# Optimization experiments

Hardware: AMD Instinct MI355X
Metric: run time of the kernel (lower is better)

The kernel has to match this reference:

```python
import jax, jax.numpy as jnp
import numpy as np

ENTITY_DIM = 128; REL_DIM = 128; D1 = 8; D2 = 16
NC = 32; K = 3
H_OUT = D1 - K + 1; W_OUT = D2 - K + 1
FEAT = NC * H_OUT * W_OUT            # 2688
NUM_ENT = 40943; NUM_REL = 474; B = 256; HID = 256
EPS = 1e-5


def _bn(x, axes):
    # torch BatchNorm train mode with default gamma=1, beta=0 (biased variance)
    m = x.mean(axes, keepdims=True)
    v = x.var(axes, keepdims=True)
    return (x - m) * jax.lax.rsqrt(v + EPS)


def setup_inputs() -> dict:
    key = jax.random.key(0)
    ks = jax.random.split(key, 12)
    s = lambda k, shp, fan: jax.random.normal(k, shp, jnp.float32) / np.float32(np.sqrt(fan))
    return {
        "e1": jax.random.randint(ks[0], (B,), 0, NUM_ENT),
        "r": jax.random.randint(ks[1], (B,), 0, NUM_REL),
        "entity_emb": s(ks[2], (NUM_ENT, ENTITY_DIM), ENTITY_DIM),
        "relation_emb": s(ks[3], (NUM_REL, REL_DIM), REL_DIM),
        "convw_w1": s(ks[4], (REL_DIM, HID), REL_DIM),
        "convw_w2": s(ks[5], (HID, NC * K * K), HID),
        "convb_w1": s(ks[6], (REL_DIM, HID), REL_DIM),
        "convb_w2": s(ks[7], (HID, NC), HID),
        "fcw_w1": s(ks[8], (REL_DIM, HID), REL_DIM),
        "fcw_w2": s(ks[9], (HID, FEAT * ENTITY_DIM), HID),
        "fcb_w1": s(ks[10], (REL_DIM, HID), REL_DIM),
        "fcb_w2": s(ks[11], (HID, ENTITY_DIM), HID),
        "b": jnp.zeros((NUM_ENT,), jnp.float32),
    }


def reference(e1, r, entity_emb, relation_emb,
              convw_w1, convw_w2, convb_w1, convb_w2,
              fcw_w1, fcw_w2, fcb_w1, fcb_w2, b):
    E1 = entity_emb[e1].reshape(B, 1, D1, D2)      # [B,1,8,16]
    R = relation_emb[r]                            # [B,128]
    E2 = entity_emb                                # [NUM_ENT,128]

    x = _bn(E1, (0, 2, 3))                         # bn0 over batch+spatial, 1 channel

    # ContextualParameterGenerator: Linear -> ReLU -> Linear (no bias, eval dropout)
    cpg = lambda w1, w2: jax.nn.relu(R @ w1) @ w2

    filt = cpg(convw_w1, convw_w2).reshape(B * NC, 1, K, K)   # per-sample conv filters
    cbias = cpg(convb_w1, convb_w2)                            # [B,NC]

    # per-sample conv2d as a grouped conv: groups=B, each group has 1 in-ch, NC out-ch
    out = jax.lax.conv_general_dilated(
        x.reshape(1, B, D1, D2), filt,
        window_strides=(1, 1), padding='VALID',
        feature_group_count=B,
        dimension_numbers=('NCHW', 'OIHW', 'NCHW'))           # [1,B*NC,6,14]
    X = out.reshape(B, NC, H_OUT, W_OUT) + cbias[:, :, None, None]
    X = jax.nn.relu(X).reshape(B, FEAT)

    fc_w = cpg(fcw_w1, fcw_w2).reshape(B, FEAT, ENTITY_DIM)   # per-sample FC weights
    X = jnp.einsum('ij,ijk->ik', X, fc_w) + cpg(fcb_w1, fcb_w2)

    X = jax.nn.relu(_bn(X, (0,)))                              # bn2 + relu
    return jax.nn.sigmoid(X @ E2.T + b)                        # [B,NUM_ENT]
```

## Files before the change

### kernel.cpp

```cpp
#include <hip/hip_runtime.h>
#include <cstdint>
#include <cstddef>

#define BATCH 256
#define ED 128
#define NC 32
#define HO 6
#define WO 14
#define FEAT 2688
#define HID 256
#define NE 40943
#define EPS 1e-5f
#define W2COLS 344064

typedef __attribute__((ext_vector_type(4))) float f32x4;
typedef __attribute__((ext_vector_type(8))) short short8;

__device__ __forceinline__ ushort f2bf(float f) {
    uint32_t u = __builtin_bit_cast(uint32_t, f);
    u = (u + 0x7FFFu + ((u >> 16) & 1u)) >> 16;
    return (ushort)u;
}

__global__ void k0_bn0(const int* __restrict__ e1, const float* __restrict__ emb,
                       float* __restrict__ stats) {
    __shared__ float s1[1024], s2[1024];
    int t = threadIdx.x;
    int i = t >> 2, p = (t & 3) * 32;
    const float* row = emb + (size_t)e1[i] * ED + p;
    float a = 0.f, b = 0.f;
#pragma unroll
    for (int q = 0; q < 32; ++q) { float v = row[q]; a += v; b += v * v; }
    s1[t] = a; s2[t] = b;
    __syncthreads();
    for (int s = 512; s > 0; s >>= 1) {
        if (t < s) { s1[t] += s1[t + s]; s2[t] += s2[t + s]; }
        __syncthreads();
    }
    if (t == 0) {
        float m = s1[0] / 32768.f;
        float v = s2[0] / 32768.f - m * m;
        stats[0] = m;
        stats[1] = rsqrtf(v + EPS);
    }
}

__global__ void k1_hidden(const int* __restrict__ r, const float* __restrict__ rel,
                          const float* __restrict__ w1a, const float* __restrict__ w1b,
                          const float* __restrict__ w1c, const float* __restrict__ w1d,
                          float* __restrict__ H) {
    int head = blockIdx.x >> 8;
    int i = blockIdx.x & 255;
    int u = threadIdx.x;
    __shared__ float R[128];
    if (u < 128) R[u] = rel[(size_t)r[i] * 128 + u];
    __syncthreads();
    const float* w1 = head == 0 ? w1a : head == 1 ? w1b : head == 2 ? w1c : w1d;
    float acc = 0.f;
#pragma unroll 8
    for (int d = 0; d < 128; ++d) acc += R[d] * w1[d * 256 + u];
    H[((size_t)head * 256 + i) * 256 + u] = fmaxf(acc, 0.f);
}

__global__ void k2_heads(const float* __restrict__ H,
                         const float* __restrict__ w2f, const float* __restrict__ w2b,
                         const float* __restrict__ w2fcb,
                         float* __restrict__ filt, float* __restrict__ cbias,
                         float* __restrict__ fcb) {
    int i = blockIdx.x;
    int t = threadIdx.x;
    __shared__ float h0[256], h1[256], h3[256];
    if (t < 256) {
        h0[t] = H[(size_t)(0 * 256 + i) * 256 + t];
        h1[t] = H[(size_t)(1 * 256 + i) * 256 + t];
        h3[t] = H[(size_t)(3 * 256 + i) * 256 + t];
    }
    __syncthreads();
    if (t < 288) {
        float a = 0.f;
#pragma unroll 8
        for (int u = 0; u < 256; ++u) a += h0[u] * w2f[u * 288 + t];
        filt[i * 288 + t] = a;
    } else if (t < 320) {
        int c = t - 288;
        float a = 0.f;
#pragma unroll 8
        for (int u = 0; u < 256; ++u) a += h1[u] * w2b[u * 32 + c];
        cbias[i * 32 + c] = a;
    } else if (t < 448) {
        int c = t - 320;
        float a = 0.f;
#pragma unroll 8
        for (int u = 0; u < 256; ++u) a += h3[u] * w2fcb[u * 128 + c];
        fcb[i * 128 + c] = a;
    }
}

__global__ void k3_conv(const int* __restrict__ e1, const float* __restrict__ emb,
                        const float* __restrict__ stats, const float* __restrict__ filt,
                        const float* __restrict__ cbias, ushort* __restrict__ Xc) {
    int i = blockIdx.x, t = threadIdx.x;
    __shared__ float x[128], f[288], cb[32];
    float mean = stats[0], rstd = stats[1];
    if (t < 128) x[t] = (emb[(size_t)e1[i] * 128 + t] - mean) * rstd;
    if (t < 32) cb[t] = cbias[i * 32 + t];
    for (int o = t; o < 288; o += 256) f[o] = filt[i * 288 + o];
    __syncthreads();
    for (int o = t; o < FEAT; o += 256) {
        int c = o / 84, rem = o % 84;
        int y = rem / 14, xw = rem % 14;
        float acc = cb[c];
        const float* fc = &f[c * 9];
#pragma unroll
        for (int dy = 0; dy < 3; ++dy)
#pragma unroll
            for (int dx = 0; dx < 3; ++dx)
                acc += x[(y + dy) * 16 + (xw + dx)] * fc[dy * 3 + dx];
        Xc[(size_t)i * FEAT + o] = f2bf(fmaxf(acc, 0.f));
    }
}

__global__ __launch_bounds__(512, 2) void k4_gemm(const ushort* __restrict__ Xc,
                                                  const float* __restrict__ W2,
                                                  float* __restrict__ T) {
    int h = blockIdx.x;
    int tid = threadIdx.x, lane = tid & 63, wave = tid >> 6;
    int l15 = lane & 15, l4 = lane >> 4;
    __shared__ __align__(16) ushort Bt[128 * 40];
    const float* Brow = W2 + (size_t)h * W2COLS;

    int kk = tid & 127;
    int jg = tid >> 7;

    f32x4 acc[2][8];
#pragma unroll
    for (int mt = 0; mt < 2; ++mt)
#pragma unroll
        for (int nt = 0; nt < 8; ++nt)
#pragma unroll
            for (int q = 0; q < 4; ++q) acc[mt][nt][q] = 0.f;

    float p[8];
#pragma unroll
    for (int q = 0; q < 8; ++q) p[q] = Brow[(size_t)(jg * 8 + q) * 128 + kk];

    for (int s = 0; s < 84; ++s) {
        __syncthreads();
        short8 w8;
#pragma unroll
        for (int q = 0; q < 8; ++q) w8[q] = (short)f2bf(p[q]);
        *(short8*)&Bt[kk * 40 + jg * 8] = w8;
        __syncthreads();
        if (s + 1 < 84) {
            int j0n = (s + 1) * 32;
#pragma unroll
            for (int q = 0; q < 8; ++q)
                p[q] = Brow[(size_t)(j0n + jg * 8 + q) * 128 + kk];
        }
        int j0 = s * 32;
        short8 bf[8];
#pragma unroll
        for (int nt = 0; nt < 8; ++nt)
            bf[nt] = *(const short8*)&Bt[(nt * 16 + l15) * 40 + l4 * 8];
        short8 af[2];
#pragma unroll
        for (int mt = 0; mt < 2; ++mt) {
            int i = wave * 32 + mt * 16 + l15;
            af[mt] = *(const short8*)(Xc + (size_t)i * FEAT + j0 + l4 * 8);
        }
#pragma unroll
        for (int mt = 0; mt < 2; ++mt)
#pragma unroll
            for (int nt = 0; nt < 8; ++nt)
                acc[mt][nt] = __builtin_amdgcn_mfma_f32_16x16x32_bf16(
                    af[mt], bf[nt], acc[mt][nt], 0, 0, 0);
    }
#pragma unroll
    for (int mt = 0; mt < 2; ++mt)
#pragma unroll
        for (int nt = 0; nt < 8; ++nt) {
            int row0 = wave * 32 + mt * 16 + l4 * 4;
            int col = nt * 16 + l15;
#pragma unroll
            for (int rr = 0; rr < 4; ++rr)
                T[((size_t)h * 256 + row0 + rr) * 128 + col] = acc[mt][nt][rr];
        }
}

__global__ void k5_stage2(const float* __restrict__ T, const float* __restrict__ Hfc,
                          const float* __restrict__ fcb, float* __restrict__ X) {
    int i = blockIdx.x, k = threadIdx.x;
    const float* hp = Hfc + (size_t)i * 256;
    const float* tp = T + (size_t)i * 128 + k;
    float acc = fcb[i * 128 + k];
#pragma unroll 8
    for (int h = 0; h < 256; ++h) acc += hp[h] * tp[(size_t)h * 32768];
    X[i * 128 + k] = acc;
}

__global__ void k6_bn2(const float* __restrict__ X, ushort* __restrict__ Xn) {
    int k = blockIdx.x;
    int i = threadIdx.x;
    __shared__ float s1[256], s2[256];
    float v = X[i * 128 + k];
    s1[i] = v; s2[i] = v * v;
    __syncthreads();
    for (int s = 128; s > 0; s >>= 1) {
        if (i < s) { s1[i] += s1[i + s]; s2[i] += s2[i + s]; }
        __syncthreads();
    }
    float m = s1[0] / 256.f;
    float var = s2[0] / 256.f - m * m;
    float rstd = rsqrtf(var + EPS);
    Xn[i * 128 + k] = f2bf(fmaxf((v - m) * rstd, 0.f));
}

__global__ __launch_bounds__(256) void k7_final(const ushort* __restrict__ Xn,
                                                const float* __restrict__ E2,
                                                const float* __restrict__ bias,
                                                float* __restrict__ out) {
    int eb = blockIdx.x * 64;
    int lane = threadIdx.x & 63, wave = threadIdx.x >> 6;
    int l15 = lane & 15, l4 = lane >> 4;
    int i0 = wave * 64;

    f32x4 acc[4][4];
#pragma unroll
    for (int mt = 0; mt < 4; ++mt)
#pragma unroll
        for (int nt = 0; nt < 4; ++nt)
#pragma unroll
            for (int q = 0; q < 4; ++q) acc[mt][nt][q] = 0.f;

#pragma unroll
    for (int ks = 0; ks < 4; ++ks) {
        int k0 = ks * 32 + l4 * 8;
        short8 a[4];
#pragma unroll
        for (int mt = 0; mt < 4; ++mt) {
            int i = i0 + mt * 16 + l15;
            a[mt] = *(const short8*)(Xn + (size_t)i * 128 + k0);
        }
        short8 b[4];
#pragma unroll
        for (int nt = 0; nt < 4; ++nt) {
            int e = eb + nt * 16 + l15;
            int ec = e < NE ? e : NE - 1;
            const float* rp = E2 + (size_t)ec * 128 + k0;
            short8 tv;
#pragma unroll
            for (int q = 0; q < 8; ++q) tv[q] = (short)f2bf(rp[q]);
            b[nt] = tv;
        }
#pragma unroll
        for (int mt = 0; mt < 4; ++mt)
#pragma unroll
            for (int nt = 0; nt < 4; ++nt)
                acc[mt][nt] = __builtin_amdgcn_mfma_f32_16x16x32_bf16(
                    a[mt], b[nt], acc[mt][nt], 0, 0, 0);
    }
#pragma unroll
    for (int nt = 0; nt < 4; ++nt) {
        int e = eb + nt * 16 + l15;
        bool ok = e < NE;
        float bb = bias[e < NE ? e : NE - 1];
#pragma unroll
        for (int mt = 0; mt < 4; ++mt) {
            int row0 = i0 + mt * 16 + l4 * 4;
#pragma unroll
            for (int rr = 0; rr < 4; ++rr) {
                float v = acc[mt][nt][rr] + bb;
                float sg = 1.f / (1.f + __expf(-v));
                if (ok) out[(size_t)(row0 + rr) * NE + e] = sg;
            }
        }
    }
}

extern "C" void kernel_launch(void* const* d_in, const int* in_sizes, int n_in,
                              void* d_out, int out_size, void* d_ws, size_t ws_size,
                              hipStream_t stream) {
    const int* e1 = (const int*)d_in[0];
    const int* r = (const int*)d_in[1];
    const float* emb = (const float*)d_in[2];
    const float* rel = (const float*)d_in[3];
    const float* convw_w1 = (const float*)d_in[4];
    const float* convw_w2 = (const float*)d_in[5];
    const float* convb_w1 = (const float*)d_in[6];
    const float* convb_w2 = (const float*)d_in[7];
    const float* fcw_w1 = (const float*)d_in[8];
    const float* fcw_w2 = (const float*)d_in[9];
    const float* fcb_w1 = (const float*)d_in[10];
    const float* fcb_w2 = (const float*)d_in[11];
    const float* bvec = (const float*)d_in[12];
    float* out = (float*)d_out;

    char* ws = (char*)d_ws;
    float* stats = (float*)(ws + 0);
    float* H = (float*)(ws + 256);
    float* filt = (float*)(ws + 1048832);
    float* cbias = (float*)(ws + 1343744);
    float* fcbv = (float*)(ws + 1376512);
    ushort* Xc = (ushort*)(ws + 1507584);
    float* T = (float*)(ws + 2883840);
    float* X = (float*)(ws + 36438272);
    ushort* Xn = (ushort*)(ws + 36569344);

    k0_bn0<<<1, 1024, 0, stream>>>(e1, emb, stats);
    k1_hidden<<<1024, 256, 0, stream>>>(r, rel, convw_w1, convb_w1, fcw_w1, fcb_w1, H);
    k2_heads<<<256, 512, 0, stream>>>(H, convw_w2, convb_w2, fcb_w2, filt, cbias, fcbv);
    k3_conv<<<256, 256, 0, stream>>>(e1, emb, stats, filt, cbias, Xc);
    k4_gemm<<<256, 512, 0, stream>>>(Xc, fcw_w2, T);
    k5_stage2<<<256, 128, 0, stream>>>(T, H + 2 * 65536, fcbv, X);
    k6_bn2<<<128, 256, 0, stream>>>(X, Xn);
    k7_final<<<640, 256, 0, stream>>>(Xn, emb, bvec, out);
}
```

Baseline: 642.1 us.

## Split k4 GEMM columns across two blocks with double-buffered LDS and deeper prefetch

The per-hidden-unit GEMM now launches two blocks per h, each handling 64 of the 128 output columns. This doubles the grid to 512 blocks so more of the GPU is filled. The B tile is double-buffered in LDS, which removes one barrier per iteration, and global loads of W2 are prefetched two steps ahead. Each block still reloads the full Xc activation tile, so A-side traffic doubles. The launch-bounds occupancy hint is raised, and a stage-2 loop gets a larger unroll.

```diff
diff --git a/kernel.cpp b/kernel.cpp
--- a/kernel.cpp
+++ b/kernel.cpp
@@ -15,6 +15,7 @@
 
 typedef __attribute__((ext_vector_type(4))) float f32x4;
 typedef __attribute__((ext_vector_type(8))) short short8;
+typedef __attribute__((ext_vector_type(4))) short short4v;
 
 __device__ __forceinline__ ushort f2bf(float f) {
     uint32_t u = __builtin_bit_cast(uint32_t, f);
@@ -120,48 +121,52 @@
     }
 }
 
-__global__ __launch_bounds__(512, 2) void k4_gemm(const ushort* __restrict__ Xc,
+__global__ __launch_bounds__(512, 4) void k4_gemm(const ushort* __restrict__ Xc,
                                                   const float* __restrict__ W2,
                                                   float* __restrict__ T) {
-    int h = blockIdx.x;
+    int h = blockIdx.x >> 1;
+    int kh = (blockIdx.x & 1) * 64;
     int tid = threadIdx.x, lane = tid & 63, wave = tid >> 6;
     int l15 = lane & 15, l4 = lane >> 4;
-    __shared__ __align__(16) ushort Bt[128 * 40];
-    const float* Brow = W2 + (size_t)h * W2COLS;
-
-    int kk = tid & 127;
-    int jg = tid >> 7;
-
-    f32x4 acc[2][8];
+    __shared__ __align__(16) ushort Bt[2][64 * 36];
+    const float* Brow = W2 + (size_t)h * W2COLS + kh;
+
+    int kk = tid & 63;
+    int jg = tid >> 6;
+    const float* src = Brow + (size_t)(jg * 4) * 128 + kk;
+
+    f32x4 acc[2][4];
 #pragma unroll
     for (int mt = 0; mt < 2; ++mt)
 #pragma unroll
-        for (int nt = 0; nt < 8; ++nt)
+        for (int nt = 0; nt < 4; ++nt)
 #pragma unroll
             for (int q = 0; q < 4; ++q) acc[mt][nt][q] = 0.f;
 
-    float p[8];
-#pragma unroll
-    for (int q = 0; q < 8; ++q) p[q] = Brow[(size_t)(jg * 8 + q) * 128 + kk];
+    float p0[4], p1[4];
+#pragma unroll
+    for (int q = 0; q < 4; ++q) p0[q] = src[(size_t)q * 128];
+#pragma unroll
+    for (int q = 0; q < 4; ++q) p1[q] = src[(size_t)(32 + q) * 128];
 
     for (int s = 0; s < 84; ++s) {
+        short4v w4;
+#pragma unroll
+        for (int q = 0; q < 4; ++q) w4[q] = (short)f2bf(p0[q]);
+        *(short4v*)&Bt[s & 1][kk * 36 + jg * 4] = w4;
         __syncthreads();
-        short8 w8;
-#pragma unroll
-        for (int q = 0; q < 8; ++q) w8[q] = (short)f2bf(p[q]);
-        *(short8*)&Bt[kk * 40 + jg * 8] = w8;
-        __syncthreads();
-        if (s + 1 < 84) {
-            int j0n = (s + 1) * 32;
-#pragma unroll
-            for (int q = 0; q < 8; ++q)
-                p[q] = Brow[(size_t)(j0n + jg * 8 + q) * 128 + kk];
+#pragma unroll
+        for (int q = 0; q < 4; ++q) p0[q] = p1[q];
+        if (s + 2 < 84) {
+            int jb = (s + 2) * 32;
+#pragma unroll
+            for (int q = 0; q < 4; ++q) p1[q] = src[(size_t)(jb + q) * 128];
         }
         int j0 = s * 32;
-        short8 bf[8];
-#pragma unroll
-        for (int nt = 0; nt < 8; ++nt)
-            bf[nt] = *(const short8*)&Bt[(nt * 16 + l15) * 40 + l4 * 8];
+        short8 bf[4];
+#pragma unroll
+        for (int nt = 0; nt < 4; ++nt)
+            bf[nt] = *(const short8*)&Bt[s & 1][(nt * 16 + l15) * 36 + l4 * 8];
         short8 af[2];
 #pragma unroll
         for (int mt = 0; mt < 2; ++mt) {
@@ -171,16 +176,16 @@
 #pragma unroll
         for (int mt = 0; mt < 2; ++mt)
 #pragma unroll
-            for (int nt = 0; nt < 8; ++nt)
+            for (int nt = 0; nt < 4; ++nt)
                 acc[mt][nt] = __builtin_amdgcn_mfma_f32_16x16x32_bf16(
                     af[mt], bf[nt], acc[mt][nt], 0, 0, 0);
     }
 #pragma unroll
     for (int mt = 0; mt < 2; ++mt)
 #pragma unroll
-        for (int nt = 0; nt < 8; ++nt) {
+        for (int nt = 0; nt < 4; ++nt) {
             int row0 = wave * 32 + mt * 16 + l4 * 4;
-            int col = nt * 16 + l15;
+            int col = kh + nt * 16 + l15;
 #pragma unroll
             for (int rr = 0; rr < 4; ++rr)
                 T[((size_t)h * 256 + row0 + rr) * 128 + col] = acc[mt][nt][rr];
@@ -193,7 +198,7 @@
     const float* hp = Hfc + (size_t)i * 256;
     const float* tp = T + (size_t)i * 128 + k;
     float acc = fcb[i * 128 + k];
-#pragma unroll 8
+#pragma unroll 16
     for (int h = 0; h < 256; ++h) acc += hp[h] * tp[(size_t)h * 32768];
     X[i * 128 + k] = acc;
 }
@@ -310,7 +315,7 @@
     k1_hidden<<<1024, 256, 0, stream>>>(r, rel, convw_w1, convb_w1, fcw_w1, fcb_w1, H);
     k2_heads<<<256, 512, 0, stream>>>(H, convw_w2, convb_w2, fcb_w2, filt, cbias, fcbv);
     k3_conv<<<256, 256, 0, stream>>>(e1, emb, stats, filt, cbias, Xc);
-    k4_gemm<<<256, 512, 0, stream>>>(Xc, fcw_w2, T);
+    k4_gemm<<<512, 512, 0, stream>>>(Xc, fcw_w2, T);
     k5_stage2<<<256, 128, 0, stream>>>(T, H + 2 * 65536, fcbv, X);
     k6_bn2<<<128, 256, 0, stream>>>(X, Xn);
     k7_final<<<640, 256, 0, stream>>>(Xn, emb, bvec, out);
```

Measured after the change: 665.3 us. 3.6% more time.
